# Performance work log

Measured on AMD Instinct MI355X. Metric: run time of the kernel, lower is better.

The kernel has to match this reference:

```python
import jax, jax.numpy as jnp
import numpy as np

VOCAB = 100000
EMB_DIM = 128
MAX_KP = 50  # config.max_num_keyphrases; lens tensors are constant-filled with this
EPS = 1e-8   # torch cosine_similarity eps


def setup_inputs() -> dict:
    key = jax.random.key(0)
    k1, k2, k3, k4 = jax.random.split(key, 4)
    B, A, K = 64, 32, 50
    batch_source = jax.random.randint(k1, (B, A, K), 0, VOCAB)
    pos_result = jax.random.randint(k2, (B, A, K), 0, VOCAB)
    neg_result = jax.random.randint(k3, (B, A, K), 0, VOCAB)
    emb_table = jax.random.normal(k4, (VOCAB + 1, EMB_DIM), dtype=jnp.float32)
    emb_table = emb_table.at[0].set(0.0)  # padding_idx=0
    return {
        "batch_source": batch_source,
        "pos_result": pos_result,
        "neg_result": neg_result,
        "emb_table": emb_table,
    }


def _embed(emb_table, idx):
    # idx: [B, A, K] -> mean-pooled [B, A, D]; denominator is the constant MAX_KP
    emb = emb_table[idx]                      # [B, A, K, D] gather (memory-bound)
    return jnp.sum(emb, axis=-2) / MAX_KP     # [B, A, D]


def _l2norm(x):
    n = jnp.sqrt(jnp.sum(x * x, axis=-1, keepdims=True))
    return x / jnp.maximum(n, EPS)


def _max_cosine(src_e, tgt_e):
    # src_e: [B, A1, D], tgt_e: [B, A2, D] -> max over all (A1, A2) pairs, per batch
    sims = jnp.einsum("bad,bcd->bac", _l2norm(src_e), _l2norm(tgt_e))  # [B, A1, A2]
    return jnp.max(sims, axis=(1, 2))  # [B]


def reference(batch_source, pos_result, neg_result, emb_table):
    src_e = _embed(emb_table, batch_source)
    pos_e = _embed(emb_table, pos_result)
    neg_e = _embed(emb_table, neg_result)
    pos_scores = _max_cosine(src_e, pos_e)  # [B]
    neg_scores = _max_cosine(src_e, neg_e)  # [B]
    x = pos_scores - neg_scores
    # BCEWithLogitsLoss with target = 1: mean(softplus(-x))
    loss = jnp.mean(jax.nn.softplus(-x))
    return loss
```

## Files before the change

### kernel.cpp

```cpp
#include <hip/hip_runtime.h>
#include <math.h>

#define BB 64
#define AA 32
#define KK 50
#define DD 128
#define MAX_KP 50
#define EPS_CS 1e-8f
#define NVEC (3 * BB * AA)
#define NCOS (8 * BB)

__device__ __forceinline__ float dot4(float4 a, float4 b) {
    return a.x * b.x + a.y * b.y + a.z * b.z + a.w * b.w;
}

__global__ __launch_bounds__(128) void embed_norm_kernel(
    const int* __restrict__ src, const int* __restrict__ pos,
    const int* __restrict__ neg, const float* __restrict__ table,
    float* __restrict__ out, unsigned* __restrict__ cnt)
{
    if (blockIdx.x == 0 && threadIdx.x == 0) cnt[0] = 0u;

    const int vec = __builtin_amdgcn_readfirstlane(
        (blockIdx.x << 1) | (threadIdx.x >> 6));
    const int t  = vec >> 11;
    const int ba = vec & 2047;
    const int* idx = ((t == 0) ? src : (t == 1) ? pos : neg) + ba * KK;

    const int lane = threadIdx.x & 63;
    const int half = lane >> 5;
    const int slot = lane & 31;

    const float4* tab4 = (const float4*)table;
    float4 acc = make_float4(0.f, 0.f, 0.f, 0.f);
    #pragma unroll
    for (int i = 0; i < KK / 2; ++i) {
        const int r0 = idx[2 * i];
        const int r1 = idx[2 * i + 1];
        const int row = half ? r1 : r0;
        const float4 v = tab4[(row << 5) + slot];
        acc.x += v.x; acc.y += v.y; acc.z += v.z; acc.w += v.w;
    }

    acc.x += __shfl_xor(acc.x, 32, 64);
    acc.y += __shfl_xor(acc.y, 32, 64);
    acc.z += __shfl_xor(acc.z, 32, 64);
    acc.w += __shfl_xor(acc.w, 32, 64);

    const float s = 1.0f / MAX_KP;
    acc.x *= s; acc.y *= s; acc.z *= s; acc.w *= s;

    float sq = dot4(acc, acc);
    #pragma unroll
    for (int off = 16; off > 0; off >>= 1) sq += __shfl_xor(sq, off, 64);

    const float inv = 1.0f / fmaxf(sqrtf(sq), EPS_CS);
    acc.x *= inv; acc.y *= inv; acc.z *= inv; acc.w *= inv;

    if (lane < 32)
        ((float4*)out)[(vec << 5) + slot] = acc;
}

__global__ __launch_bounds__(256) void cosine_loss_kernel(
    const float* __restrict__ embs, float* __restrict__ part ,
    unsigned* __restrict__ cnt, float* __restrict__ out)
{
    const int blk  = blockIdx.x;
    const int b    = blk >> 3;
    const int q    = blk & 7;
    const int tens = q >> 2;
    const int ih   = (q >> 1) & 1;
    const int jh   = q & 1;
    const int tid  = threadIdx.x;

    __shared__ float s_src[16][DD + 4];
    __shared__ float s_tgt[16][DD + 4];

    const float4* src4 = (const float4*)(embs + ((long)b * AA + ih * 16) * DD);
    const float4* tgt4 = (const float4*)(embs +
                          ((long)(BB + tens * BB + b) * AA + jh * 16) * DD);

    for (int i = tid; i < 16 * DD / 4; i += 256) {
        const int r = i >> 5, c = i & 31;
        *(float4*)&s_src[r][c * 4] = src4[i];
        *(float4*)&s_tgt[r][c * 4] = tgt4[i];
    }
    __syncthreads();

    const int si = tid >> 4;
    const int j  = tid & 15;

    float dsum = 0.f;
    #pragma unroll 8
    for (int d0 = 0; d0 < DD; d0 += 4)
        dsum += dot4(*(const float4*)&s_src[si][d0],
                     *(const float4*)&s_tgt[j][d0]);

    float m = dsum;
    #pragma unroll
    for (int off = 32; off > 0; off >>= 1) m = fmaxf(m, __shfl_xor(m, off, 64));
    __shared__ float sm[4];
    __shared__ int s_win;
    if ((tid & 63) == 0) sm[tid >> 6] = m;
    __syncthreads();

    if (tid == 0) {
        const float bm = fmaxf(fmaxf(sm[0], sm[1]), fmaxf(sm[2], sm[3]));
        __hip_atomic_store(&part[blk], bm, __ATOMIC_RELAXED,
                           __HIP_MEMORY_SCOPE_AGENT);
        const unsigned old = __hip_atomic_fetch_add(
            cnt, 1u, __ATOMIC_ACQ_REL, __HIP_MEMORY_SCOPE_AGENT);
        s_win = (old == NCOS - 1);
    }
    __syncthreads();
    if (!s_win) return;

    if (tid < BB) {
        float v[8];
        v[0] = __hip_atomic_load(&part[tid * 8 + 0], __ATOMIC_ACQUIRE,
                                 __HIP_MEMORY_SCOPE_AGENT);
        #pragma unroll
        for (int k = 1; k < 8; ++k)
            v[k] = __hip_atomic_load(&part[tid * 8 + k], __ATOMIC_RELAXED,
                                     __HIP_MEMORY_SCOPE_AGENT);
        const float P = fmaxf(fmaxf(v[0], v[1]), fmaxf(v[2], v[3]));
        const float N = fmaxf(fmaxf(v[4], v[5]), fmaxf(v[6], v[7]));
        const float x = P - N;
        float l = (x >= 0.f) ? log1pf(expf(-x)) : (-x + log1pf(expf(x)));
        #pragma unroll
        for (int off = 32; off > 0; off >>= 1) l += __shfl_xor(l, off, 64);
        if (tid == 0) out[0] = l * (1.0f / BB);
    }
}

extern "C" void kernel_launch(void* const* d_in, const int* in_sizes, int n_in,
                              void* d_out, int out_size, void* d_ws, size_t ws_size,
                              hipStream_t stream) {
    const int*   batch_source = (const int*)d_in[0];
    const int*   pos_result   = (const int*)d_in[1];
    const int*   neg_result   = (const int*)d_in[2];
    const float* emb_table    = (const float*)d_in[3];
    float* out = (float*)d_out;

    float*    embs = (float*)d_ws;
    float*    part = embs + 3L * BB * AA * DD;
    unsigned* cnt  = (unsigned*)(part + NCOS);

    embed_norm_kernel<<<NVEC / 2, 128, 0, stream>>>(
        batch_source, pos_result, neg_result, emb_table, embs, cnt);
    cosine_loss_kernel<<<NCOS, 256, 0, stream>>>(embs, part, cnt, out);
}
```

Before: 40.44 us.

## Use one 512-thread block per batch for both pos and neg cosine max

The cosine kernel drops from 512 blocks of 256 threads (one quadrant per block) to 64 blocks of 512 threads, one per batch. Each thread computes four dot products against pos and neg while reusing its src row from shared memory, and softplus is evaluated per batch before the final reduction. This cuts redundant loads of src and the number of atomic handoffs. The cost is less parallelism, only 64 blocks, and more shared memory per block.

```diff
diff --git a/kernel.cpp b/kernel.cpp
--- a/kernel.cpp
+++ b/kernel.cpp
@@ -8,7 +8,6 @@
 #define MAX_KP 50
 #define EPS_CS 1e-8f
 #define NVEC (3 * BB * AA)
-#define NCOS (8 * BB)
 
 __device__ __forceinline__ float dot4(float4 a, float4 b) {
     return a.x * b.x + a.y * b.y + a.z * b.z + a.w * b.w;
@@ -61,72 +60,74 @@
         ((float4*)out)[(vec << 5) + slot] = acc;
 }
 
-__global__ __launch_bounds__(256) void cosine_loss_kernel(
-    const float* __restrict__ embs, float* __restrict__ part ,
+__global__ __launch_bounds__(512) void cosine_loss_kernel(
+    const float* __restrict__ embs, float* __restrict__ per_batch,
     unsigned* __restrict__ cnt, float* __restrict__ out)
 {
-    const int blk  = blockIdx.x;
-    const int b    = blk >> 3;
-    const int q    = blk & 7;
-    const int tens = q >> 2;
-    const int ih   = (q >> 1) & 1;
-    const int jh   = q & 1;
-    const int tid  = threadIdx.x;
+    const int b   = blockIdx.x;
+    const int tid = threadIdx.x;
 
-    __shared__ float s_src[16][DD + 4];
-    __shared__ float s_tgt[16][DD + 4];
+    __shared__ float s_src[AA][DD + 4];
+    __shared__ float s_pos[AA][DD + 4];
+    __shared__ float s_neg[AA][DD + 4];
 
-    const float4* src4 = (const float4*)(embs + ((long)b * AA + ih * 16) * DD);
-    const float4* tgt4 = (const float4*)(embs +
-                          ((long)(BB + tens * BB + b) * AA + jh * 16) * DD);
+    const float4* src4 = (const float4*)(embs + (long)b * AA * DD);
+    const float4* pos4 = (const float4*)(embs + (long)(BB + b) * AA * DD);
+    const float4* neg4 = (const float4*)(embs + (long)(2 * BB + b) * AA * DD);
 
-    for (int i = tid; i < 16 * DD / 4; i += 256) {
+    for (int i = tid; i < AA * DD / 4; i += 512) {
         const int r = i >> 5, c = i & 31;
         *(float4*)&s_src[r][c * 4] = src4[i];
-        *(float4*)&s_tgt[r][c * 4] = tgt4[i];
+        *(float4*)&s_pos[r][c * 4] = pos4[i];
+        *(float4*)&s_neg[r][c * 4] = neg4[i];
     }
     __syncthreads();
 
-    const int si = tid >> 4;
-    const int j  = tid & 15;
+    const int i  = tid >> 4;
+    const int j0 = tid & 15;
 
-    float dsum = 0.f;
+    float p0 = 0.f, p1 = 0.f, n0 = 0.f, n1 = 0.f;
     #pragma unroll 8
-    for (int d0 = 0; d0 < DD; d0 += 4)
-        dsum += dot4(*(const float4*)&s_src[si][d0],
-                     *(const float4*)&s_tgt[j][d0]);
+    for (int d0 = 0; d0 < DD; d0 += 4) {
+        const float4 a  = *(const float4*)&s_src[i][d0];
+        const float4 pA = *(const float4*)&s_pos[j0][d0];
+        const float4 pB = *(const float4*)&s_pos[j0 + 16][d0];
+        const float4 nA = *(const float4*)&s_neg[j0][d0];
+        const float4 nB = *(const float4*)&s_neg[j0 + 16][d0];
+        p0 += dot4(a, pA); p1 += dot4(a, pB);
+        n0 += dot4(a, nA); n1 += dot4(a, nB);
+    }
+    float pmax = fmaxf(p0, p1);
+    float nmax = fmaxf(n0, n1);
 
-    float m = dsum;
     #pragma unroll
-    for (int off = 32; off > 0; off >>= 1) m = fmaxf(m, __shfl_xor(m, off, 64));
-    __shared__ float sm[4];
+    for (int off = 32; off > 0; off >>= 1) {
+        pmax = fmaxf(pmax, __shfl_xor(pmax, off, 64));
+        nmax = fmaxf(nmax, __shfl_xor(nmax, off, 64));
+    }
+    __shared__ float sp[8], sn[8];
     __shared__ int s_win;
-    if ((tid & 63) == 0) sm[tid >> 6] = m;
+    if ((tid & 63) == 0) { sp[tid >> 6] = pmax; sn[tid >> 6] = nmax; }
     __syncthreads();
 
     if (tid == 0) {
-        const float bm = fmaxf(fmaxf(sm[0], sm[1]), fmaxf(sm[2], sm[3]));
-        __hip_atomic_store(&part[blk], bm, __ATOMIC_RELAXED,
+        float P = sp[0], N = sn[0];
+        #pragma unroll
+        for (int w = 1; w < 8; ++w) { P = fmaxf(P, sp[w]); N = fmaxf(N, sn[w]); }
+        const float x = P - N;
+        const float l = (x >= 0.f) ? log1pf(expf(-x)) : (-x + log1pf(expf(x)));
+        __hip_atomic_store(&per_batch[b], l, __ATOMIC_RELAXED,
                            __HIP_MEMORY_SCOPE_AGENT);
         const unsigned old = __hip_atomic_fetch_add(
             cnt, 1u, __ATOMIC_ACQ_REL, __HIP_MEMORY_SCOPE_AGENT);
-        s_win = (old == NCOS - 1);
+        s_win = (old == BB - 1);
     }
     __syncthreads();
     if (!s_win) return;
 
     if (tid < BB) {
-        float v[8];
-        v[0] = __hip_atomic_load(&part[tid * 8 + 0], __ATOMIC_ACQUIRE,
-                                 __HIP_MEMORY_SCOPE_AGENT);
-        #pragma unroll
-        for (int k = 1; k < 8; ++k)
-            v[k] = __hip_atomic_load(&part[tid * 8 + k], __ATOMIC_RELAXED,
-                                     __HIP_MEMORY_SCOPE_AGENT);
-        const float P = fmaxf(fmaxf(v[0], v[1]), fmaxf(v[2], v[3]));
-        const float N = fmaxf(fmaxf(v[4], v[5]), fmaxf(v[6], v[7]));
-        const float x = P - N;
-        float l = (x >= 0.f) ? log1pf(expf(-x)) : (-x + log1pf(expf(x)));
+        float l = __hip_atomic_load(&per_batch[tid], __ATOMIC_ACQUIRE,
+                                    __HIP_MEMORY_SCOPE_AGENT);
         #pragma unroll
         for (int off = 32; off > 0; off >>= 1) l += __shfl_xor(l, off, 64);
         if (tid == 0) out[0] = l * (1.0f / BB);
@@ -142,11 +143,11 @@
     const float* emb_table    = (const float*)d_in[3];
     float* out = (float*)d_out;
 
-    float*    embs = (float*)d_ws;
-    float*    part = embs + 3L * BB * AA * DD;
-    unsigned* cnt  = (unsigned*)(part + NCOS);
+    float*    embs      = (float*)d_ws;
+    float*    per_batch = embs + 3L * BB * AA * DD;
+    unsigned* cnt       = (unsigned*)(per_batch + BB);
 
     embed_norm_kernel<<<NVEC / 2, 128, 0, stream>>>(
         batch_source, pos_result, neg_result, emb_table, embs, cnt);
-    cosine_loss_kernel<<<NCOS, 256, 0, stream>>>(embs, part, cnt, out);
+    cosine_loss_kernel<<<BB, 512, 0, stream>>>(embs, per_batch, cnt, out);
 }
```

New measurement: 35.22 us. -12.9%, faster.
